# Optimization experiments

Measured on AMD Instinct MI355X. Metric: run time of the kernel, lower is better.

Reference implementation:

```python
import jax, jax.numpy as jnp
import numpy as np

D = 64      # n_embd (== head_size in this module)
H = 8       # n_heads
B = 4
T = 2048    # seq len == block_size
EPS = 1e-5


def layernorm(x, g, b):
    mu = jnp.mean(x, axis=-1, keepdims=True)
    var = jnp.mean(jnp.square(x - mu), axis=-1, keepdims=True)
    return (x - mu) * jax.lax.rsqrt(var + EPS) * g + b


def setup_inputs() -> dict:
    key = jax.random.key(0)
    ks = jax.random.split(key, 16)
    s = 1.0 / np.sqrt(D)
    inp = {
        'inputs': jax.random.normal(ks[0], (B, T, D), jnp.float32),
        # per-head QKV linears: weight [H, D, D] (in, out), bias [H, D]
        'Wq': jax.random.uniform(ks[1], (H, D, D), jnp.float32, -s, s),
        'bq': jax.random.uniform(ks[2], (H, D), jnp.float32, -s, s),
        'Wk': jax.random.uniform(ks[3], (H, D, D), jnp.float32, -s, s),
        'bk': jax.random.uniform(ks[4], (H, D), jnp.float32, -s, s),
        'Wv': jax.random.uniform(ks[5], (H, D, D), jnp.float32, -s, s),
        'bv': jax.random.uniform(ks[6], (H, D), jnp.float32, -s, s),
        # projection: Linear(H*D -> D)
        'Wp': jax.random.uniform(ks[7], (H * D, D), jnp.float32, -1/np.sqrt(H*D), 1/np.sqrt(H*D)),
        'bp': jax.random.uniform(ks[8], (D,), jnp.float32, -1/np.sqrt(H*D), 1/np.sqrt(H*D)),
        # FFN: D -> 4D -> D
        'W1': jax.random.uniform(ks[9], (D, 4 * D), jnp.float32, -s, s),
        'b1': jax.random.uniform(ks[10], (4 * D,), jnp.float32, -s, s),
        'W2': jax.random.uniform(ks[11], (4 * D, D), jnp.float32, -1/np.sqrt(4*D), 1/np.sqrt(4*D)),
        'b2': jax.random.uniform(ks[12], (D,), jnp.float32, -1/np.sqrt(4*D), 1/np.sqrt(4*D)),
        'g1': jnp.ones((D,), jnp.float32), 'be1': jnp.zeros((D,), jnp.float32),
        'g2': jnp.ones((D,), jnp.float32), 'be2': jnp.zeros((D,), jnp.float32),
    }
    return inp


def reference(inputs, Wq, bq, Wk, bk, Wv, bv, Wp, bp, W1, b1, W2, b2, g1, be1, g2, be2):
    x = inputs
    # per-head full-width QKV: [H, B, T, D]
    q = jnp.einsum('btd,hde->hbte', x, Wq) + bq[:, None, None, :]
    k = jnp.einsum('btd,hde->hbte', x, Wk) + bk[:, None, None, :]
    v = jnp.einsum('btd,hde->hbte', x, Wv) + bv[:, None, None, :]
    # unscaled scores (module has no 1/sqrt(d) scaling)
    scores = jnp.einsum('hbte,hbse->hbts', q, k)  # [H, B, T, T]
    causal = jnp.tril(jnp.ones((T, T), bool))
    scores = jnp.where(causal, scores, -jnp.inf)
    attn = jax.nn.softmax(scores, axis=-1)
    out = jnp.einsum('hbts,hbse->hbte', attn, v)  # [H, B, T, D]
    # torch.cat over heads along last dim -> [B, T, H*D]
    cat = jnp.transpose(out, (1, 2, 0, 3)).reshape(B, T, H * D)
    attn_out = cat @ Wp + bp
    h1 = layernorm(x + attn_out, g1, be1)
    ffn = jax.nn.relu(h1 @ W1 + b1) @ W2 + b2
    return layernorm(h1 + ffn, g2, be2)
```

## Files before the change

### kernel.cpp

```cpp
#include <hip/hip_runtime.h>
#include <hip/hip_bf16.h>
#include <stdint.h>

#define Dd 64
#define Hh 8
#define Bb 4
#define Tt 2048
#define NT (Bb * Tt)

typedef __attribute__((ext_vector_type(4))) float f32x4;
typedef __attribute__((ext_vector_type(8))) __bf16 bf16x8;
typedef __attribute__((ext_vector_type(8))) uint16_t u16x8;

__device__ __forceinline__ uint16_t f2bf_fast(float f) {
    union { __bf16 h; uint16_t u; } c; c.h = (__bf16)f; return c.u;
}

#define SWZ(row, k)   ((row) * 72  + ((k) ^ ((((row) >> 3) & 7) << 3)))
#define PSZ(q, k)     ((q)  * 72  + ((k) ^ ((((q)  >> 2) & 3) << 3)))
#define W2SWZ(col, k) ((col) * 264 + ((k) ^ ((((col) >> 3) & 7) << 3)))
#define WPSWZ(col, k) ((col) * 520 + ((k) ^ ((((col) >> 3) & 7) << 3)))

__global__ __launch_bounds__(256) void qkv_kernel(
    const float* __restrict__ x,
    const float* __restrict__ Wq, const float* __restrict__ bq,
    const float* __restrict__ Wk, const float* __restrict__ bk,
    const float* __restrict__ Wv, const float* __restrict__ bv,
    uint16_t* __restrict__ qb, uint16_t* __restrict__ kb, uint16_t* __restrict__ vb)
{
    __shared__ uint16_t WtF[64 * 72];
    const int rt = blockIdx.x, h = blockIdx.y, m = blockIdx.z;
    const float* W    = (m == 0) ? Wq : (m == 1) ? Wk : Wv;
    const float* bias = (m == 0) ? bq : (m == 1) ? bk : bv;
    uint16_t*    out  = (m == 0) ? qb : (m == 1) ? kb : vb;
    const int t = threadIdx.x, lane = t & 63, w = t >> 6;
    const int l15 = lane & 15, g = lane >> 4;

#pragma unroll
    for (int p = 0; p < 4; ++p) {
        int idx = p * 256 + t;
        int r = idx >> 4, c4 = (idx & 15) * 4;
        f32x4 wv = *(const f32x4*)&W[(size_t)(h * 64 + r) * 64 + c4];
#pragma unroll
        for (int j = 0; j < 4; ++j) WtF[SWZ(c4 + j, r)] = f2bf_fast(wv[j]);
    }

    const int row = rt * 64 + w * 16 + l15;
    union { u16x8 u; bf16x8 b; } a0, a1;
    {
        f32x4 x0 = *(const f32x4*)&x[(size_t)row * 64 + g * 8];
        f32x4 x1 = *(const f32x4*)&x[(size_t)row * 64 + g * 8 + 4];
        f32x4 x2 = *(const f32x4*)&x[(size_t)row * 64 + 32 + g * 8];
        f32x4 x3 = *(const f32x4*)&x[(size_t)row * 64 + 32 + g * 8 + 4];
#pragma unroll
        for (int j = 0; j < 4; ++j) {
            a0.u[j] = f2bf_fast(x0[j]); a0.u[4 + j] = f2bf_fast(x1[j]);
            a1.u[j] = f2bf_fast(x2[j]); a1.u[4 + j] = f2bf_fast(x3[j]);
        }
    }
    __syncthreads();

    f32x4 acc[4] = {};
#pragma unroll
    for (int ct = 0; ct < 4; ++ct) {
        bf16x8 b0 = *(const bf16x8*)&WtF[SWZ(ct * 16 + l15, g * 8)];
        bf16x8 b1 = *(const bf16x8*)&WtF[SWZ(ct * 16 + l15, 32 + g * 8)];
        acc[ct] = __builtin_amdgcn_mfma_f32_16x16x32_bf16(a0.b, b0, acc[ct], 0, 0, 0);
        acc[ct] = __builtin_amdgcn_mfma_f32_16x16x32_bf16(a1.b, b1, acc[ct], 0, 0, 0);
    }
#pragma unroll
    for (int ct = 0; ct < 4; ++ct) {
        float bb = bias[h * 64 + ct * 16 + l15];
#pragma unroll
        for (int rr = 0; rr < 4; ++rr) {
            int orow = rt * 64 + w * 16 + g * 4 + rr;
            out[((size_t)h * NT + orow) * 64 + ct * 16 + l15] =
                f2bf_fast(acc[ct][rr] + bb);
        }
    }
}

__global__ __launch_bounds__(256) void attn_kernel3(
    const uint16_t* __restrict__ qb, const uint16_t* __restrict__ kb,
    const uint16_t* __restrict__ vb, uint16_t* __restrict__ cat)
{
    __shared__ uint16_t KsF[2][64 * 72];
    __shared__ uint16_t VtF[2][64 * 72];
    __shared__ uint16_t PsF[4][16 * 72];
    const int pairid = blockIdx.x, h = blockIdx.y, b = blockIdx.z;
    const int t = threadIdx.x, lane = t & 63, wave = t >> 6;
    const int l15 = lane & 15, g = lane >> 4;
    const size_t base = ((size_t)h * NT + (size_t)b * Tt) * 64;
    const uint16_t* Qh = qb + base;
    const uint16_t* Kh = kb + base;
    const uint16_t* Vh = vb + base;
    const int rS = t >> 3, cS = (t & 7) * 8;

    for (int ph = 0; ph < 2; ++ph) {
        const int qt = ph ? (31 - pairid) : pairid;
        bf16x8 aq0, aq1;
        {
            int qrow = qt * 64 + wave * 16 + l15;
            aq0 = *(const bf16x8*)&Qh[(size_t)qrow * 64 + g * 8];
            aq1 = *(const bf16x8*)&Qh[(size_t)qrow * 64 + 32 + g * 8];
        }
        f32x4 o[4] = {};
        float m_run[4], l_run[4];
#pragma unroll
        for (int r = 0; r < 4; ++r) { m_run[r] = -INFINITY; l_run[r] = 0.f; }

        __syncthreads();
        {
            u16x8 k0 = *(const u16x8*)&Kh[(size_t)(rS) * 64 + cS];
            u16x8 k1 = *(const u16x8*)&Kh[(size_t)(32 + rS) * 64 + cS];
            u16x8 v0 = *(const u16x8*)&Vh[(size_t)(rS) * 64 + cS];
            u16x8 v1 = *(const u16x8*)&Vh[(size_t)(32 + rS) * 64 + cS];
            *(u16x8*)&KsF[0][SWZ(rS, cS)] = k0;
            *(u16x8*)&KsF[0][SWZ(32 + rS, cS)] = k1;
#pragma unroll
            for (int j = 0; j < 8; ++j) {
                VtF[0][SWZ(cS + j, rS)] = v0[j];
                VtF[0][SWZ(cS + j, 32 + rS)] = v1[j];
            }
        }
        __syncthreads();

        for (int kv = 0; kv <= qt; ++kv) {
            const int cur = kv & 1;
            const bool pf = kv < qt;
            u16x8 pk0, pk1, pv0, pv1;
            if (pf) {
                int kr = (kv + 1) * 64;
                pk0 = *(const u16x8*)&Kh[(size_t)(kr + rS) * 64 + cS];
                pk1 = *(const u16x8*)&Kh[(size_t)(kr + 32 + rS) * 64 + cS];
                pv0 = *(const u16x8*)&Vh[(size_t)(kr + rS) * 64 + cS];
                pv1 = *(const u16x8*)&Vh[(size_t)(kr + 32 + rS) * 64 + cS];
            }
            f32x4 s[4];
#pragma unroll
            for (int kt = 0; kt < 4; ++kt) {
                bf16x8 bk0 = *(const bf16x8*)&KsF[cur][SWZ(kt * 16 + l15, g * 8)];
                bf16x8 bk1 = *(const bf16x8*)&KsF[cur][SWZ(kt * 16 + l15, 32 + g * 8)];
                f32x4 z = {};
                z = __builtin_amdgcn_mfma_f32_16x16x32_bf16(aq0, bk0, z, 0, 0, 0);
                z = __builtin_amdgcn_mfma_f32_16x16x32_bf16(aq1, bk1, z, 0, 0, 0);
                s[kt] = z;
            }
            if (kv == qt) {
#pragma unroll
                for (int kt = 0; kt < 4; ++kt) {
                    int key = kt * 16 + l15;
#pragma unroll
                    for (int r = 0; r < 4; ++r) {
                        int qr = wave * 16 + g * 4 + r;
                        if (key > qr) s[kt][r] = -INFINITY;
                    }
                }
            }
            float mt[4];
#pragma unroll
            for (int r = 0; r < 4; ++r) {
                mt[r] = fmaxf(fmaxf(s[0][r], s[1][r]), fmaxf(s[2][r], s[3][r]));
                mt[r] = fmaxf(mt[r], __shfl_xor(mt[r], 1));
                mt[r] = fmaxf(mt[r], __shfl_xor(mt[r], 2));
                mt[r] = fmaxf(mt[r], __shfl_xor(mt[r], 4));
                mt[r] = fmaxf(mt[r], __shfl_xor(mt[r], 8));
            }
            bool need = false;
#pragma unroll
            for (int r = 0; r < 4; ++r) need |= (mt[r] > m_run[r] + 8.f);
            if (__any((int)need)) {
#pragma unroll
                for (int r = 0; r < 4; ++r) {
                    float mnew = fmaxf(m_run[r], mt[r]);
                    float a = __expf(m_run[r] - mnew);
                    m_run[r] = mnew;
                    l_run[r] *= a;
                    o[0][r] *= a; o[1][r] *= a; o[2][r] *= a; o[3][r] *= a;
                }
            }
            float ls[4];
#pragma unroll
            for (int r = 0; r < 4; ++r) {
                float sum = 0.f;
#pragma unroll
                for (int kt = 0; kt < 4; ++kt) {
                    float p = __expf(s[kt][r] - m_run[r]);
                    s[kt][r] = p;
                    sum += p;
                }
                ls[r] = sum;
            }
#pragma unroll
            for (int r = 0; r < 4; ++r) {
                ls[r] += __shfl_xor(ls[r], 1);
                ls[r] += __shfl_xor(ls[r], 2);
                ls[r] += __shfl_xor(ls[r], 4);
                ls[r] += __shfl_xor(ls[r], 8);
                l_run[r] += ls[r];
            }
#pragma unroll
            for (int kt = 0; kt < 4; ++kt)
#pragma unroll
                for (int r = 0; r < 4; ++r)
                    PsF[wave][PSZ(g * 4 + r, kt * 16 + l15)] = f2bf_fast(s[kt][r]);
#pragma unroll
            for (int c = 0; c < 2; ++c) {
                bf16x8 ap = *(const bf16x8*)&PsF[wave][PSZ(l15, c * 32 + g * 8)];
#pragma unroll
                for (int dt = 0; dt < 4; ++dt) {
                    bf16x8 bv = *(const bf16x8*)&VtF[cur][SWZ(dt * 16 + l15, c * 32 + g * 8)];
                    o[dt] = __builtin_amdgcn_mfma_f32_16x16x32_bf16(ap, bv, o[dt], 0, 0, 0);
                }
            }
            if (pf) {
                *(u16x8*)&KsF[cur ^ 1][SWZ(rS, cS)] = pk0;
                *(u16x8*)&KsF[cur ^ 1][SWZ(32 + rS, cS)] = pk1;
#pragma unroll
                for (int j = 0; j < 8; ++j) {
                    VtF[cur ^ 1][SWZ(cS + j, rS)] = pv0[j];
                    VtF[cur ^ 1][SWZ(cS + j, 32 + rS)] = pv1[j];
                }
                __syncthreads();
            }
        }
        float inv[4];
#pragma unroll
        for (int r = 0; r < 4; ++r) inv[r] = 1.f / l_run[r];
#pragma unroll
        for (int dt = 0; dt < 4; ++dt)
#pragma unroll
            for (int r = 0; r < 4; ++r) {
                int row = qt * 64 + wave * 16 + g * 4 + r;
                cat[((size_t)b * Tt + row) * (Hh * 64) + h * 64 + dt * 16 + l15] =
                    f2bf_fast(o[dt][r] * inv[r]);
            }
    }
}

__global__ __launch_bounds__(256) void proj_ln1_mfma(
    const uint16_t* __restrict__ cat, const float* __restrict__ Wp,
    const float* __restrict__ bp, const float* __restrict__ x,
    const float* __restrict__ g1, const float* __restrict__ be1,
    float* __restrict__ h1, uint16_t* __restrict__ h1b)
{
    __shared__ uint16_t WptF[64 * 520];
    const int rt = blockIdx.x;
    const int t = threadIdx.x, lane = t & 63, w = t >> 6;
    const int l15 = lane & 15, g = lane >> 4;
#pragma unroll
    for (int p = 0; p < 32; ++p) {
        int idx = p * 256 + t;
        int r = idx >> 4, c4 = (idx & 15) * 4;
        f32x4 wv = *(const f32x4*)&Wp[(size_t)r * 64 + c4];
#pragma unroll
        for (int j = 0; j < 4; ++j) WptF[WPSWZ(c4 + j, r)] = f2bf_fast(wv[j]);
    }
    __syncthreads();
    const int arow = rt * 64 + w * 16 + l15;
    f32x4 acc[4] = {};
#pragma unroll
    for (int kt = 0; kt < 16; ++kt) {
        bf16x8 a = *(const bf16x8*)&cat[(size_t)arow * 512 + kt * 32 + g * 8];
#pragma unroll
        for (int ct = 0; ct < 4; ++ct) {
            bf16x8 bfr = *(const bf16x8*)&WptF[WPSWZ(ct * 16 + l15, kt * 32 + g * 8)];
            acc[ct] = __builtin_amdgcn_mfma_f32_16x16x32_bf16(a, bfr, acc[ct], 0, 0, 0);
        }
    }
    float bpv[4], g1v[4], b1v[4];
#pragma unroll
    for (int ct = 0; ct < 4; ++ct) {
        bpv[ct] = bp[ct * 16 + l15];
        g1v[ct] = g1[ct * 16 + l15];
        b1v[ct] = be1[ct * 16 + l15];
    }
#pragma unroll
    for (int rr = 0; rr < 4; ++rr) {
        int drow = rt * 64 + w * 16 + g * 4 + rr;
        float s[4], sum = 0.f;
#pragma unroll
        for (int ct = 0; ct < 4; ++ct) {
            s[ct] = acc[ct][rr] + bpv[ct] + x[(size_t)drow * 64 + ct * 16 + l15];
            sum += s[ct];
        }
        sum += __shfl_xor(sum, 1); sum += __shfl_xor(sum, 2);
        sum += __shfl_xor(sum, 4); sum += __shfl_xor(sum, 8);
        float mu = sum * (1.f / 64.f);
        float v = 0.f;
#pragma unroll
        for (int ct = 0; ct < 4; ++ct) { s[ct] -= mu; v += s[ct] * s[ct]; }
        v += __shfl_xor(v, 1); v += __shfl_xor(v, 2);
        v += __shfl_xor(v, 4); v += __shfl_xor(v, 8);
        float rstd = rsqrtf(v * (1.f / 64.f) + 1e-5f);
#pragma unroll
        for (int ct = 0; ct < 4; ++ct) {
            float hv = s[ct] * rstd * g1v[ct] + b1v[ct];
            h1 [(size_t)drow * 64 + ct * 16 + l15] = hv;
            h1b[(size_t)drow * 64 + ct * 16 + l15] = f2bf_fast(hv);
        }
    }
}

__global__ __launch_bounds__(256) void ffn_mfma(
    const uint16_t* __restrict__ h1b, const float* __restrict__ h1,
    const float* __restrict__ W1, const float* __restrict__ b1,
    const float* __restrict__ W2, const float* __restrict__ b2,
    const float* __restrict__ g2, const float* __restrict__ be2,
    float* __restrict__ out)
{
    __shared__ uint16_t W1t[256 * 72];
    __shared__ uint16_t W2t[64 * 264];
    __shared__ uint16_t hidS[4][16 * 264];
    const int rt = blockIdx.x;
    const int t = threadIdx.x, lane = t & 63, w = t >> 6;
    const int l15 = lane & 15, g = lane >> 4;
#pragma unroll
    for (int p = 0; p < 16; ++p) {
        int idx = p * 256 + t;
        int r = idx >> 6, c4 = (idx & 63) * 4;
        f32x4 wv = *(const f32x4*)&W1[(size_t)r * 256 + c4];
#pragma unroll
        for (int j = 0; j < 4; ++j) W1t[SWZ(c4 + j, r)] = f2bf_fast(wv[j]);
    }
#pragma unroll
    for (int p = 0; p < 16; ++p) {
        int idx = p * 256 + t;
        int r = idx >> 4, c4 = (idx & 15) * 4;
        f32x4 wv = *(const f32x4*)&W2[(size_t)r * 64 + c4];
#pragma unroll
        for (int j = 0; j < 4; ++j) W2t[W2SWZ(c4 + j, r)] = f2bf_fast(wv[j]);
    }
    __syncthreads();
    const int arow = rt * 64 + w * 16 + l15;
    f32x4 acc1[16] = {};
#pragma unroll
    for (int ks = 0; ks < 2; ++ks) {
        bf16x8 a = *(const bf16x8*)&h1b[(size_t)arow * 64 + ks * 32 + g * 8];
#pragma unroll
        for (int ct = 0; ct < 16; ++ct) {
            bf16x8 bfr = *(const bf16x8*)&W1t[SWZ(ct * 16 + l15, ks * 32 + g * 8)];
            acc1[ct] = __builtin_amdgcn_mfma_f32_16x16x32_bf16(a, bfr, acc1[ct], 0, 0, 0);
        }
    }
#pragma unroll
    for (int ct = 0; ct < 16; ++ct) {
        float bb = b1[ct * 16 + l15];
#pragma unroll
        for (int rr = 0; rr < 4; ++rr)
            hidS[w][(g * 4 + rr) * 264 + ct * 16 + l15] =
                f2bf_fast(fmaxf(acc1[ct][rr] + bb, 0.f));
    }
    f32x4 acc2[4] = {};
#pragma unroll
    for (int ks = 0; ks < 8; ++ks) {
        bf16x8 a = *(const bf16x8*)&hidS[w][l15 * 264 + ks * 32 + g * 8];
#pragma unroll
        for (int ct = 0; ct < 4; ++ct) {
            bf16x8 bfr = *(const bf16x8*)&W2t[W2SWZ(ct * 16 + l15, ks * 32 + g * 8)];
            acc2[ct] = __builtin_amdgcn_mfma_f32_16x16x32_bf16(a, bfr, acc2[ct], 0, 0, 0);
        }
    }
    float b2v[4], g2v[4], be2v[4];
#pragma unroll
    for (int ct = 0; ct < 4; ++ct) {
        b2v[ct]  = b2[ct * 16 + l15];
        g2v[ct]  = g2[ct * 16 + l15];
        be2v[ct] = be2[ct * 16 + l15];
    }
#pragma unroll
    for (int rr = 0; rr < 4; ++rr) {
        int drow = rt * 64 + w * 16 + g * 4 + rr;
        float s[4], sum = 0.f;
#pragma unroll
        for (int ct = 0; ct < 4; ++ct) {
            s[ct] = acc2[ct][rr] + b2v[ct] + h1[(size_t)drow * 64 + ct * 16 + l15];
            sum += s[ct];
        }
        sum += __shfl_xor(sum, 1); sum += __shfl_xor(sum, 2);
        sum += __shfl_xor(sum, 4); sum += __shfl_xor(sum, 8);
        float mu = sum * (1.f / 64.f);
        float v = 0.f;
#pragma unroll
        for (int ct = 0; ct < 4; ++ct) { s[ct] -= mu; v += s[ct] * s[ct]; }
        v += __shfl_xor(v, 1); v += __shfl_xor(v, 2);
        v += __shfl_xor(v, 4); v += __shfl_xor(v, 8);
        float rstd = rsqrtf(v * (1.f / 64.f) + 1e-5f);
#pragma unroll
        for (int ct = 0; ct < 4; ++ct)
            out[(size_t)drow * 64 + ct * 16 + l15] =
                s[ct] * rstd * g2v[ct] + be2v[ct];
    }
}

extern "C" void kernel_launch(void* const* d_in, const int* in_sizes, int n_in,
                              void* d_out, int out_size, void* d_ws, size_t ws_size,
                              hipStream_t stream)
{
    (void)in_sizes; (void)n_in; (void)out_size; (void)ws_size;
    const float* x   = (const float*)d_in[0];
    const float* Wq  = (const float*)d_in[1];
    const float* bq  = (const float*)d_in[2];
    const float* Wk  = (const float*)d_in[3];
    const float* bk  = (const float*)d_in[4];
    const float* Wv  = (const float*)d_in[5];
    const float* bv  = (const float*)d_in[6];
    const float* Wp  = (const float*)d_in[7];
    const float* bp  = (const float*)d_in[8];
    const float* W1  = (const float*)d_in[9];
    const float* b1  = (const float*)d_in[10];
    const float* W2  = (const float*)d_in[11];
    const float* b2  = (const float*)d_in[12];
    const float* g1  = (const float*)d_in[13];
    const float* be1 = (const float*)d_in[14];
    const float* g2  = (const float*)d_in[15];
    const float* be2 = (const float*)d_in[16];
    float* outp = (float*)d_out;

    char* w = (char*)d_ws;
    uint16_t* qb  = (uint16_t*)w;
    uint16_t* kb  = qb + (size_t)Hh * NT * 64;
    uint16_t* vb  = kb + (size_t)Hh * NT * 64;
    uint16_t* cat = vb + (size_t)Hh * NT * 64;
    float*    h1  = (float*)(cat + (size_t)NT * 512);
    uint16_t* h1b = (uint16_t*)(h1 + (size_t)NT * 64);

    qkv_kernel<<<dim3(NT / 64, Hh, 3), dim3(256), 0, stream>>>(
        x, Wq, bq, Wk, bk, Wv, bv, qb, kb, vb);
    attn_kernel3<<<dim3(16, Hh, Bb), dim3(256), 0, stream>>>(qb, kb, vb, cat);
    proj_ln1_mfma<<<dim3(NT / 64), dim3(256), 0, stream>>>(
        cat, Wp, bp, x, g1, be1, h1, h1b);
    ffn_mfma<<<dim3(NT / 64), dim3(256), 0, stream>>>(
        h1b, h1, W1, b1, W2, b2, g2, be2, outp);
}
```

Baseline: 192.2 us.

## Restructure attention with register-resident P and fuse projection, LN and FFN

Attention now uses 128-thread blocks on 32-row query tiles, with 1024 blocks in an XCD-aware order. It computes S transposed so the probabilities stay in registers as the MFMA A operand, which removes the LDS round trip for P. The projection, first layernorm and FFN are merged into one tail kernel that keeps h1 in registers and LDS instead of writing it to global memory. Weight conversion to swizzled bf16 moves into a separate setup kernel, and the tail kernel reads those weights straight from global memory. The tail kernel therefore no longer stages weights in LDS per block, and it relies on cache hits for its weight fragment loads.

```diff
diff --git a/kernel.cpp b/kernel.cpp
--- a/kernel.cpp
+++ b/kernel.cpp
@@ -11,15 +11,54 @@
 typedef __attribute__((ext_vector_type(4))) float f32x4;
 typedef __attribute__((ext_vector_type(8))) __bf16 bf16x8;
 typedef __attribute__((ext_vector_type(8))) uint16_t u16x8;
+typedef __attribute__((ext_vector_type(4))) uint16_t u16x4;
 
 __device__ __forceinline__ uint16_t f2bf_fast(float f) {
     union { __bf16 h; uint16_t u; } c; c.h = (__bf16)f; return c.u;
 }
+__device__ __forceinline__ uint32_t pkbf(float a, float b) {
+    return (uint32_t)f2bf_fast(a) | ((uint32_t)f2bf_fast(b) << 16);
+}
 
 #define SWZ(row, k)   ((row) * 72  + ((k) ^ ((((row) >> 3) & 7) << 3)))
 #define PSZ(q, k)     ((q)  * 72  + ((k) ^ ((((q)  >> 2) & 3) << 3)))
+#define HSZ(q, k)     ((q)  * 264 + ((k) ^ ((((q)  >> 2) & 3) << 3)))
 #define W2SWZ(col, k) ((col) * 264 + ((k) ^ ((((col) >> 3) & 7) << 3)))
 #define WPSWZ(col, k) ((col) * 520 + ((k) ^ ((((col) >> 3) & 7) << 3)))
+
+__global__ __launch_bounds__(256) void setup_kernel(
+    const float* __restrict__ Wp, const float* __restrict__ W1,
+    const float* __restrict__ W2,
+    uint16_t* __restrict__ WptS, uint16_t* __restrict__ W1g,
+    uint16_t* __restrict__ W2g)
+{
+    const int bid = blockIdx.x, t = threadIdx.x;
+    if (bid < 8) {
+        const int j = bid;
+#pragma unroll
+        for (int p = 0; p < 16; ++p) {
+            int idx = p * 256 + t;
+            int col = idx & 63, k = j * 64 + (idx >> 6);
+            WptS[WPSWZ(col, k)] = f2bf_fast(Wp[(size_t)k * 64 + col]);
+        }
+    } else if (bid < 12) {
+        const int j = bid - 8;
+#pragma unroll
+        for (int p = 0; p < 16; ++p) {
+            int e = j * 4096 + p * 256 + t;
+            int col = e & 255, k = e >> 8;
+            W1g[SWZ(col, k)] = f2bf_fast(W1[(size_t)k * 256 + col]);
+        }
+    } else {
+        const int j = bid - 12;
+#pragma unroll
+        for (int p = 0; p < 16; ++p) {
+            int e = j * 4096 + p * 256 + t;
+            int col = e & 63, k = e >> 6;
+            W2g[W2SWZ(col, k)] = f2bf_fast(W2[(size_t)k * 64 + col]);
+        }
+    }
+}
 
 __global__ __launch_bounds__(256) void qkv_kernel(
     const float* __restrict__ x,
@@ -44,7 +83,6 @@
 #pragma unroll
         for (int j = 0; j < 4; ++j) WtF[SWZ(c4 + j, r)] = f2bf_fast(wv[j]);
     }
-
     const int row = rt * 64 + w * 16 + l15;
     union { u16x8 u; bf16x8 b; } a0, a1;
     {
@@ -80,61 +118,61 @@
     }
 }
 
-__global__ __launch_bounds__(256) void attn_kernel3(
+__global__ __launch_bounds__(128) void attn_kernel5(
     const uint16_t* __restrict__ qb, const uint16_t* __restrict__ kb,
     const uint16_t* __restrict__ vb, uint16_t* __restrict__ cat)
 {
     __shared__ uint16_t KsF[2][64 * 72];
     __shared__ uint16_t VtF[2][64 * 72];
-    __shared__ uint16_t PsF[4][16 * 72];
-    const int pairid = blockIdx.x, h = blockIdx.y, b = blockIdx.z;
-    const int t = threadIdx.x, lane = t & 63, wave = t >> 6;
+    const int bid = blockIdx.x;
+    const int lbid = (bid & 7) * 128 + (bid >> 3);
+    const int pairid = lbid & 31;
+    const int hb = lbid >> 5;
+    const int h = hb & 7, b = hb >> 3;
+    const int t = threadIdx.x, lane = t & 63, w = t >> 6;
     const int l15 = lane & 15, g = lane >> 4;
     const size_t base = ((size_t)h * NT + (size_t)b * Tt) * 64;
     const uint16_t* Qh = qb + base;
     const uint16_t* Kh = kb + base;
     const uint16_t* Vh = vb + base;
-    const int rS = t >> 3, cS = (t & 7) * 8;
 
     for (int ph = 0; ph < 2; ++ph) {
-        const int qt = ph ? (31 - pairid) : pairid;
+        const int qt32 = ph ? (63 - pairid) : pairid;
         bf16x8 aq0, aq1;
         {
-            int qrow = qt * 64 + wave * 16 + l15;
+            int qrow = qt32 * 32 + w * 16 + l15;
             aq0 = *(const bf16x8*)&Qh[(size_t)qrow * 64 + g * 8];
             aq1 = *(const bf16x8*)&Qh[(size_t)qrow * 64 + 32 + g * 8];
         }
         f32x4 o[4] = {};
-        float m_run[4], l_run[4];
-#pragma unroll
-        for (int r = 0; r < 4; ++r) { m_run[r] = -INFINITY; l_run[r] = 0.f; }
+        float m_run = -INFINITY, l_run = 0.f;
 
         __syncthreads();
-        {
-            u16x8 k0 = *(const u16x8*)&Kh[(size_t)(rS) * 64 + cS];
-            u16x8 k1 = *(const u16x8*)&Kh[(size_t)(32 + rS) * 64 + cS];
-            u16x8 v0 = *(const u16x8*)&Vh[(size_t)(rS) * 64 + cS];
-            u16x8 v1 = *(const u16x8*)&Vh[(size_t)(32 + rS) * 64 + cS];
-            *(u16x8*)&KsF[0][SWZ(rS, cS)] = k0;
-            *(u16x8*)&KsF[0][SWZ(32 + rS, cS)] = k1;
-#pragma unroll
-            for (int j = 0; j < 8; ++j) {
-                VtF[0][SWZ(cS + j, rS)] = v0[j];
-                VtF[0][SWZ(cS + j, 32 + rS)] = v1[j];
-            }
+#pragma unroll
+        for (int i = 0; i < 4; ++i) {
+            int slot = i * 128 + t;
+            int r = slot >> 3, c8 = (slot & 7) * 8;
+            u16x8 kk = *(const u16x8*)&Kh[(size_t)r * 64 + c8];
+            u16x8 vv = *(const u16x8*)&Vh[(size_t)r * 64 + c8];
+            *(u16x8*)&KsF[0][SWZ(r, c8)] = kk;
+#pragma unroll
+            for (int j = 0; j < 8; ++j) VtF[0][SWZ(c8 + j, r)] = vv[j];
         }
         __syncthreads();
 
-        for (int kv = 0; kv <= qt; ++kv) {
+        const int nkv = (qt32 >> 1) + 1;
+        for (int kv = 0; kv < nkv; ++kv) {
             const int cur = kv & 1;
-            const bool pf = kv < qt;
-            u16x8 pk0, pk1, pv0, pv1;
+            const bool pf = (kv + 1) < nkv;
+            u16x8 pK[4], pV[4];
             if (pf) {
-                int kr = (kv + 1) * 64;
-                pk0 = *(const u16x8*)&Kh[(size_t)(kr + rS) * 64 + cS];
-                pk1 = *(const u16x8*)&Kh[(size_t)(kr + 32 + rS) * 64 + cS];
-                pv0 = *(const u16x8*)&Vh[(size_t)(kr + rS) * 64 + cS];
-                pv1 = *(const u16x8*)&Vh[(size_t)(kr + 32 + rS) * 64 + cS];
+#pragma unroll
+                for (int i = 0; i < 4; ++i) {
+                    int slot = i * 128 + t;
+                    int r = (kv + 1) * 64 + (slot >> 3), c8 = (slot & 7) * 8;
+                    pK[i] = *(const u16x8*)&Kh[(size_t)r * 64 + c8];
+                    pV[i] = *(const u16x8*)&Vh[(size_t)r * 64 + c8];
+                }
             }
             f32x4 s[4];
 #pragma unroll
@@ -142,129 +180,119 @@
                 bf16x8 bk0 = *(const bf16x8*)&KsF[cur][SWZ(kt * 16 + l15, g * 8)];
                 bf16x8 bk1 = *(const bf16x8*)&KsF[cur][SWZ(kt * 16 + l15, 32 + g * 8)];
                 f32x4 z = {};
-                z = __builtin_amdgcn_mfma_f32_16x16x32_bf16(aq0, bk0, z, 0, 0, 0);
-                z = __builtin_amdgcn_mfma_f32_16x16x32_bf16(aq1, bk1, z, 0, 0, 0);
+                z = __builtin_amdgcn_mfma_f32_16x16x32_bf16(bk0, aq0, z, 0, 0, 0);
+                z = __builtin_amdgcn_mfma_f32_16x16x32_bf16(bk1, aq1, z, 0, 0, 0);
                 s[kt] = z;
             }
-            if (kv == qt) {
-#pragma unroll
-                for (int kt = 0; kt < 4; ++kt) {
-                    int key = kt * 16 + l15;
-#pragma unroll
-                    for (int r = 0; r < 4; ++r) {
-                        int qr = wave * 16 + g * 4 + r;
-                        if (key > qr) s[kt][r] = -INFINITY;
-                    }
+            if (kv == nkv - 1) {
+                int qlocal = (qt32 & 1) * 32 + w * 16 + l15;
+#pragma unroll
+                for (int kt = 0; kt < 4; ++kt)
+#pragma unroll
+                    for (int rj = 0; rj < 4; ++rj)
+                        if (kt * 16 + g * 4 + rj > qlocal) s[kt][rj] = -INFINITY;
+            }
+            float mt = s[0][0];
+#pragma unroll
+            for (int kt = 0; kt < 4; ++kt)
+#pragma unroll
+                for (int rj = 0; rj < 4; ++rj) mt = fmaxf(mt, s[kt][rj]);
+            mt = fmaxf(mt, __shfl_xor(mt, 16));
+            mt = fmaxf(mt, __shfl_xor(mt, 32));
+            if (__any((int)(mt > m_run + 8.f))) {
+                float mnew = fmaxf(m_run, mt);
+                float alpha = __expf(m_run - mnew);
+                m_run = mnew;
+                l_run *= alpha;
+                float a0 = __shfl(alpha, g * 4 + 0);
+                float a1 = __shfl(alpha, g * 4 + 1);
+                float a2 = __shfl(alpha, g * 4 + 2);
+                float a3 = __shfl(alpha, g * 4 + 3);
+#pragma unroll
+                for (int dt = 0; dt < 4; ++dt) {
+                    o[dt][0] *= a0; o[dt][1] *= a1; o[dt][2] *= a2; o[dt][3] *= a3;
                 }
             }
-            float mt[4];
-#pragma unroll
-            for (int r = 0; r < 4; ++r) {
-                mt[r] = fmaxf(fmaxf(s[0][r], s[1][r]), fmaxf(s[2][r], s[3][r]));
-                mt[r] = fmaxf(mt[r], __shfl_xor(mt[r], 1));
-                mt[r] = fmaxf(mt[r], __shfl_xor(mt[r], 2));
-                mt[r] = fmaxf(mt[r], __shfl_xor(mt[r], 4));
-                mt[r] = fmaxf(mt[r], __shfl_xor(mt[r], 8));
-            }
-            bool need = false;
-#pragma unroll
-            for (int r = 0; r < 4; ++r) need |= (mt[r] > m_run[r] + 8.f);
-            if (__any((int)need)) {
-#pragma unroll
-                for (int r = 0; r < 4; ++r) {
-                    float mnew = fmaxf(m_run[r], mt[r]);
-                    float a = __expf(m_run[r] - mnew);
-                    m_run[r] = mnew;
-                    l_run[r] *= a;
-                    o[0][r] *= a; o[1][r] *= a; o[2][r] *= a; o[3][r] *= a;
+            float ls = 0.f;
+#pragma unroll
+            for (int kt = 0; kt < 4; ++kt)
+#pragma unroll
+                for (int rj = 0; rj < 4; ++rj) {
+                    float p = __expf(s[kt][rj] - m_run);
+                    s[kt][rj] = p;
+                    ls += p;
                 }
-            }
-            float ls[4];
-#pragma unroll
-            for (int r = 0; r < 4; ++r) {
-                float sum = 0.f;
-#pragma unroll
-                for (int kt = 0; kt < 4; ++kt) {
-                    float p = __expf(s[kt][r] - m_run[r]);
-                    s[kt][r] = p;
-                    sum += p;
+            ls += __shfl_xor(ls, 16);
+            ls += __shfl_xor(ls, 32);
+            l_run += ls;
+            union { uint32_t wd[4]; bf16x8 v; } ap0, ap1;
+            ap0.wd[0] = pkbf(s[0][0], s[0][1]); ap0.wd[1] = pkbf(s[0][2], s[0][3]);
+            ap0.wd[2] = pkbf(s[1][0], s[1][1]); ap0.wd[3] = pkbf(s[1][2], s[1][3]);
+            ap1.wd[0] = pkbf(s[2][0], s[2][1]); ap1.wd[1] = pkbf(s[2][2], s[2][3]);
+            ap1.wd[2] = pkbf(s[3][0], s[3][1]); ap1.wd[3] = pkbf(s[3][2], s[3][3]);
+#pragma unroll
+            for (int c = 0; c < 2; ++c) {
+                const bf16x8 ap = c ? ap1.v : ap0.v;
+#pragma unroll
+                for (int dt = 0; dt < 4; ++dt) {
+                    union { u16x4 q[2]; bf16x8 v; } bb;
+                    bb.q[0] = *(const u16x4*)&VtF[cur][SWZ(dt * 16 + l15, c * 32 + g * 4)];
+                    bb.q[1] = *(const u16x4*)&VtF[cur][SWZ(dt * 16 + l15, c * 32 + 16 + g * 4)];
+                    o[dt] = __builtin_amdgcn_mfma_f32_16x16x32_bf16(ap, bb.v, o[dt], 0, 0, 0);
                 }
-                ls[r] = sum;
-            }
-#pragma unroll
-            for (int r = 0; r < 4; ++r) {
-                ls[r] += __shfl_xor(ls[r], 1);
-                ls[r] += __shfl_xor(ls[r], 2);
-                ls[r] += __shfl_xor(ls[r], 4);
-                ls[r] += __shfl_xor(ls[r], 8);
-                l_run[r] += ls[r];
-            }
-#pragma unroll
-            for (int kt = 0; kt < 4; ++kt)
-#pragma unroll
-                for (int r = 0; r < 4; ++r)
-                    PsF[wave][PSZ(g * 4 + r, kt * 16 + l15)] = f2bf_fast(s[kt][r]);
-#pragma unroll
-            for (int c = 0; c < 2; ++c) {
-                bf16x8 ap = *(const bf16x8*)&PsF[wave][PSZ(l15, c * 32 + g * 8)];
-#pragma unroll
-                for (int dt = 0; dt < 4; ++dt) {
-                    bf16x8 bv = *(const bf16x8*)&VtF[cur][SWZ(dt * 16 + l15, c * 32 + g * 8)];
-                    o[dt] = __builtin_amdgcn_mfma_f32_16x16x32_bf16(ap, bv, o[dt], 0, 0, 0);
-                }
             }
             if (pf) {
-                *(u16x8*)&KsF[cur ^ 1][SWZ(rS, cS)] = pk0;
-                *(u16x8*)&KsF[cur ^ 1][SWZ(32 + rS, cS)] = pk1;
-#pragma unroll
-                for (int j = 0; j < 8; ++j) {
-                    VtF[cur ^ 1][SWZ(cS + j, rS)] = pv0[j];
-                    VtF[cur ^ 1][SWZ(cS + j, 32 + rS)] = pv1[j];
+#pragma unroll
+                for (int i = 0; i < 4; ++i) {
+                    int slot = i * 128 + t;
+                    int r = slot >> 3, c8 = (slot & 7) * 8;
+                    *(u16x8*)&KsF[cur ^ 1][SWZ(r, c8)] = pK[i];
+#pragma unroll
+                    for (int j = 0; j < 8; ++j) VtF[cur ^ 1][SWZ(c8 + j, r)] = pV[i][j];
                 }
                 __syncthreads();
             }
         }
-        float inv[4];
-#pragma unroll
-        for (int r = 0; r < 4; ++r) inv[r] = 1.f / l_run[r];
-#pragma unroll
-        for (int dt = 0; dt < 4; ++dt)
-#pragma unroll
-            for (int r = 0; r < 4; ++r) {
-                int row = qt * 64 + wave * 16 + g * 4 + r;
-                cat[((size_t)b * Tt + row) * (Hh * 64) + h * 64 + dt * 16 + l15] =
-                    f2bf_fast(o[dt][r] * inv[r]);
-            }
-    }
-}
-
-__global__ __launch_bounds__(256) void proj_ln1_mfma(
-    const uint16_t* __restrict__ cat, const float* __restrict__ Wp,
-    const float* __restrict__ bp, const float* __restrict__ x,
+        float inv = 1.f / l_run;
+        float i0 = __shfl(inv, g * 4 + 0);
+        float i1 = __shfl(inv, g * 4 + 1);
+        float i2 = __shfl(inv, g * 4 + 2);
+        float i3 = __shfl(inv, g * 4 + 3);
+#pragma unroll
+        for (int dt = 0; dt < 4; ++dt) {
+            int rowb = qt32 * 32 + w * 16 + g * 4;
+            size_t cb = ((size_t)b * Tt + rowb) * 512 + h * 64 + dt * 16 + l15;
+            cat[cb]         = f2bf_fast(o[dt][0] * i0);
+            cat[cb + 512]   = f2bf_fast(o[dt][1] * i1);
+            cat[cb + 1024]  = f2bf_fast(o[dt][2] * i2);
+            cat[cb + 1536]  = f2bf_fast(o[dt][3] * i3);
+        }
+    }
+}
+
+__global__ __launch_bounds__(128) void tail_kernel(
+    const uint16_t* __restrict__ cat, const uint16_t* __restrict__ WptS,
+    const uint16_t* __restrict__ W1g, const uint16_t* __restrict__ W2g,
+    const float* __restrict__ bp, const float* __restrict__ b1,
+    const float* __restrict__ b2, const float* __restrict__ x,
     const float* __restrict__ g1, const float* __restrict__ be1,
-    float* __restrict__ h1, uint16_t* __restrict__ h1b)
+    const float* __restrict__ g2, const float* __restrict__ be2,
+    float* __restrict__ out)
 {
-    __shared__ uint16_t WptF[64 * 520];
+    __shared__ uint16_t h1S[2][16 * 72];
+    __shared__ uint16_t hidS[2][16 * 264];
     const int rt = blockIdx.x;
     const int t = threadIdx.x, lane = t & 63, w = t >> 6;
     const int l15 = lane & 15, g = lane >> 4;
-#pragma unroll
-    for (int p = 0; p < 32; ++p) {
-        int idx = p * 256 + t;
-        int r = idx >> 4, c4 = (idx & 15) * 4;
-        f32x4 wv = *(const f32x4*)&Wp[(size_t)r * 64 + c4];
-#pragma unroll
-        for (int j = 0; j < 4; ++j) WptF[WPSWZ(c4 + j, r)] = f2bf_fast(wv[j]);
-    }
-    __syncthreads();
-    const int arow = rt * 64 + w * 16 + l15;
+    const int arow = rt * 32 + w * 16 + l15;
+
     f32x4 acc[4] = {};
 #pragma unroll
     for (int kt = 0; kt < 16; ++kt) {
         bf16x8 a = *(const bf16x8*)&cat[(size_t)arow * 512 + kt * 32 + g * 8];
 #pragma unroll
         for (int ct = 0; ct < 4; ++ct) {
-            bf16x8 bfr = *(const bf16x8*)&WptF[WPSWZ(ct * 16 + l15, kt * 32 + g * 8)];
+            bf16x8 bfr = *(const bf16x8*)&WptS[WPSWZ(ct * 16 + l15, kt * 32 + g * 8)];
             acc[ct] = __builtin_amdgcn_mfma_f32_16x16x32_bf16(a, bfr, acc[ct], 0, 0, 0);
         }
     }
@@ -275,9 +303,10 @@
         g1v[ct] = g1[ct * 16 + l15];
         b1v[ct] = be1[ct * 16 + l15];
     }
+    float hv[4][4];
 #pragma unroll
     for (int rr = 0; rr < 4; ++rr) {
-        int drow = rt * 64 + w * 16 + g * 4 + rr;
+        int drow = rt * 32 + w * 16 + g * 4 + rr;
         float s[4], sum = 0.f;
 #pragma unroll
         for (int ct = 0; ct < 4; ++ct) {
@@ -295,70 +324,34 @@
         float rstd = rsqrtf(v * (1.f / 64.f) + 1e-5f);
 #pragma unroll
         for (int ct = 0; ct < 4; ++ct) {
-            float hv = s[ct] * rstd * g1v[ct] + b1v[ct];
-            h1 [(size_t)drow * 64 + ct * 16 + l15] = hv;
-            h1b[(size_t)drow * 64 + ct * 16 + l15] = f2bf_fast(hv);
-        }
-    }
-}
-
-__global__ __launch_bounds__(256) void ffn_mfma(
-    const uint16_t* __restrict__ h1b, const float* __restrict__ h1,
-    const float* __restrict__ W1, const float* __restrict__ b1,
-    const float* __restrict__ W2, const float* __restrict__ b2,
-    const float* __restrict__ g2, const float* __restrict__ be2,
-    float* __restrict__ out)
-{
-    __shared__ uint16_t W1t[256 * 72];
-    __shared__ uint16_t W2t[64 * 264];
-    __shared__ uint16_t hidS[4][16 * 264];
-    const int rt = blockIdx.x;
-    const int t = threadIdx.x, lane = t & 63, w = t >> 6;
-    const int l15 = lane & 15, g = lane >> 4;
-#pragma unroll
-    for (int p = 0; p < 16; ++p) {
-        int idx = p * 256 + t;
-        int r = idx >> 6, c4 = (idx & 63) * 4;
-        f32x4 wv = *(const f32x4*)&W1[(size_t)r * 256 + c4];
-#pragma unroll
-        for (int j = 0; j < 4; ++j) W1t[SWZ(c4 + j, r)] = f2bf_fast(wv[j]);
-    }
-#pragma unroll
-    for (int p = 0; p < 16; ++p) {
-        int idx = p * 256 + t;
-        int r = idx >> 4, c4 = (idx & 15) * 4;
-        f32x4 wv = *(const f32x4*)&W2[(size_t)r * 64 + c4];
-#pragma unroll
-        for (int j = 0; j < 4; ++j) W2t[W2SWZ(c4 + j, r)] = f2bf_fast(wv[j]);
-    }
-    __syncthreads();
-    const int arow = rt * 64 + w * 16 + l15;
-    f32x4 acc1[16] = {};
-#pragma unroll
-    for (int ks = 0; ks < 2; ++ks) {
-        bf16x8 a = *(const bf16x8*)&h1b[(size_t)arow * 64 + ks * 32 + g * 8];
-#pragma unroll
-        for (int ct = 0; ct < 16; ++ct) {
-            bf16x8 bfr = *(const bf16x8*)&W1t[SWZ(ct * 16 + l15, ks * 32 + g * 8)];
-            acc1[ct] = __builtin_amdgcn_mfma_f32_16x16x32_bf16(a, bfr, acc1[ct], 0, 0, 0);
-        }
-    }
-#pragma unroll
-    for (int ct = 0; ct < 16; ++ct) {
-        float bb = b1[ct * 16 + l15];
+            float h = s[ct] * rstd * g1v[ct] + b1v[ct];
+            hv[ct][rr] = h;
+            h1S[w][PSZ(g * 4 + rr, ct * 16 + l15)] = f2bf_fast(h);
+        }
+    }
+    bf16x8 ha0 = *(const bf16x8*)&h1S[w][PSZ(l15, g * 8)];
+    bf16x8 ha1 = *(const bf16x8*)&h1S[w][PSZ(l15, 32 + g * 8)];
+#pragma unroll
+    for (int nt = 0; nt < 16; ++nt) {
+        f32x4 a1c = {};
+        bf16x8 w10 = *(const bf16x8*)&W1g[SWZ(nt * 16 + l15, g * 8)];
+        bf16x8 w11 = *(const bf16x8*)&W1g[SWZ(nt * 16 + l15, 32 + g * 8)];
+        a1c = __builtin_amdgcn_mfma_f32_16x16x32_bf16(ha0, w10, a1c, 0, 0, 0);
+        a1c = __builtin_amdgcn_mfma_f32_16x16x32_bf16(ha1, w11, a1c, 0, 0, 0);
+        float bb1 = b1[nt * 16 + l15];
 #pragma unroll
         for (int rr = 0; rr < 4; ++rr)
-            hidS[w][(g * 4 + rr) * 264 + ct * 16 + l15] =
-                f2bf_fast(fmaxf(acc1[ct][rr] + bb, 0.f));
+            hidS[w][HSZ(g * 4 + rr, nt * 16 + l15)] =
+                f2bf_fast(fmaxf(a1c[rr] + bb1, 0.f));
     }
     f32x4 acc2[4] = {};
 #pragma unroll
     for (int ks = 0; ks < 8; ++ks) {
-        bf16x8 a = *(const bf16x8*)&hidS[w][l15 * 264 + ks * 32 + g * 8];
+        bf16x8 hfr = *(const bf16x8*)&hidS[w][HSZ(l15, ks * 32 + g * 8)];
 #pragma unroll
         for (int ct = 0; ct < 4; ++ct) {
-            bf16x8 bfr = *(const bf16x8*)&W2t[W2SWZ(ct * 16 + l15, ks * 32 + g * 8)];
-            acc2[ct] = __builtin_amdgcn_mfma_f32_16x16x32_bf16(a, bfr, acc2[ct], 0, 0, 0);
+            bf16x8 w2f = *(const bf16x8*)&W2g[W2SWZ(ct * 16 + l15, ks * 32 + g * 8)];
+            acc2[ct] = __builtin_amdgcn_mfma_f32_16x16x32_bf16(hfr, w2f, acc2[ct], 0, 0, 0);
         }
     }
     float b2v[4], g2v[4], be2v[4];
@@ -370,11 +363,11 @@
     }
 #pragma unroll
     for (int rr = 0; rr < 4; ++rr) {
-        int drow = rt * 64 + w * 16 + g * 4 + rr;
+        int drow = rt * 32 + w * 16 + g * 4 + rr;
         float s[4], sum = 0.f;
 #pragma unroll
         for (int ct = 0; ct < 4; ++ct) {
-            s[ct] = acc2[ct][rr] + b2v[ct] + h1[(size_t)drow * 64 + ct * 16 + l15];
+            s[ct] = acc2[ct][rr] + b2v[ct] + hv[ct][rr];
             sum += s[ct];
         }
         sum += __shfl_xor(sum, 1); sum += __shfl_xor(sum, 2);
@@ -418,18 +411,18 @@
     float* outp = (float*)d_out;
 
     char* w = (char*)d_ws;
-    uint16_t* qb  = (uint16_t*)w;
-    uint16_t* kb  = qb + (size_t)Hh * NT * 64;
-    uint16_t* vb  = kb + (size_t)Hh * NT * 64;
-    uint16_t* cat = vb + (size_t)Hh * NT * 64;
-    float*    h1  = (float*)(cat + (size_t)NT * 512);
-    uint16_t* h1b = (uint16_t*)(h1 + (size_t)NT * 64);
-
+    uint16_t* qb   = (uint16_t*)w;
+    uint16_t* kb   = qb + (size_t)Hh * NT * 64;
+    uint16_t* vb   = kb + (size_t)Hh * NT * 64;
+    uint16_t* cat  = vb + (size_t)Hh * NT * 64;
+    uint16_t* WptS = cat + (size_t)NT * 512;
+    uint16_t* W1g  = WptS + 33280;
+    uint16_t* W2g  = W1g + 18432;
+
+    setup_kernel<<<dim3(16), dim3(256), 0, stream>>>(Wp, W1, W2, WptS, W1g, W2g);
     qkv_kernel<<<dim3(NT / 64, Hh, 3), dim3(256), 0, stream>>>(
         x, Wq, bq, Wk, bk, Wv, bv, qb, kb, vb);
-    attn_kernel3<<<dim3(16, Hh, Bb), dim3(256), 0, stream>>>(qb, kb, vb, cat);
-    proj_ln1_mfma<<<dim3(NT / 64), dim3(256), 0, stream>>>(
-        cat, Wp, bp, x, g1, be1, h1, h1b);
-    ffn_mfma<<<dim3(NT / 64), dim3(256), 0, stream>>>(
-        h1b, h1, W1, b1, W2, b2, g2, be2, outp);
-}
+    attn_kernel5<<<dim3(1024), dim3(128), 0, stream>>>(qb, kb, vb, cat);
+    tail_kernel<<<dim3(256), dim3(128), 0, stream>>>(
+        cat, WptS, W1g, W2g, bp, b1, b2, x, g1, be1, g2, be2, outp);
+}
```

Result: faster. 175.2 us (-8.8%).
